# Optimization experiments

Measured on AMD Instinct MI355X. Metric: run time of the kernel, lower is better.

## Reference

```python
import jax, jax.numpy as jnp
from jax import lax
import numpy as np

B, C_IN, HW = 4096, 3, 32
D = 256          # feature/output dim
E = 16           # num experts
H = 1024         # expert hidden dim
K = 2            # top-k
NC = 1000        # num classes


def _conv(x, w, b):
    # x: NCHW, w: OIHW, stride 1, SAME padding
    y = lax.conv_general_dilated(x, w, (1, 1), 'SAME',
                                 dimension_numbers=('NCHW', 'OIHW', 'NCHW'))
    return y + b[None, :, None, None]


def _maxpool2(x):
    return lax.reduce_window(x, -jnp.inf, lax.max, (1, 1, 2, 2), (1, 1, 2, 2), 'VALID')


def setup_inputs() -> dict:
    key = jax.random.key(0)
    ks = jax.random.split(key, 16)
    s = lambda *sh: 1.0 / np.sqrt(sh[-2] if len(sh) > 1 else sh[0])
    inp = {
        'x':       jax.random.normal(ks[0], (B, C_IN, HW, HW), jnp.float32),
        'conv1_w': jax.random.normal(ks[1], (32, 3, 3, 3), jnp.float32) * 0.1,
        'conv1_b': jnp.zeros((32,), jnp.float32),
        'conv2_w': jax.random.normal(ks[2], (64, 32, 3, 3), jnp.float32) * 0.05,
        'conv2_b': jnp.zeros((64,), jnp.float32),
        'conv3_w': jax.random.normal(ks[3], (128, 64, 3, 3), jnp.float32) * 0.04,
        'conv3_b': jnp.zeros((128,), jnp.float32),
        'fc_w':    jax.random.normal(ks[4], (128 * 4 * 4, D), jnp.float32) * (1.0 / np.sqrt(2048)),
        'fc_b':    jnp.zeros((D,), jnp.float32),
        'gate_w':  jax.random.normal(ks[5], (D, E), jnp.float32) * (1.0 / np.sqrt(D)),
        'gate_b':  jnp.zeros((E,), jnp.float32),
        'e_w1':    jax.random.normal(ks[6], (E, D, H), jnp.float32) * (1.0 / np.sqrt(D)),
        'e_b1':    jnp.zeros((E, H), jnp.float32),
        'e_w2':    jax.random.normal(ks[7], (E, H, D), jnp.float32) * (1.0 / np.sqrt(H)),
        'e_b2':    jnp.zeros((E, D), jnp.float32),
        'ln_g':    jnp.ones((D,), jnp.float32),
        'ln_b':    jnp.zeros((D,), jnp.float32),
        'out_w':   jax.random.normal(ks[8], (D, NC), jnp.float32) * (1.0 / np.sqrt(D)),
        'out_b':   jnp.zeros((NC,), jnp.float32),
    }
    return inp


def reference(x, conv1_w, conv1_b, conv2_w, conv2_b, conv3_w, conv3_b,
              fc_w, fc_b, gate_w, gate_b, e_w1, e_b1, e_w2, e_b2,
              ln_g, ln_b, out_w, out_b):
    # --- CNN feature extractor: conv -> maxpool -> relu, x3 ---
    h = jax.nn.relu(_maxpool2(_conv(x, conv1_w, conv1_b)))   # [B,32,16,16]
    h = jax.nn.relu(_maxpool2(_conv(h, conv2_w, conv2_b)))   # [B,64,8,8]
    h = jax.nn.relu(_maxpool2(_conv(h, conv3_w, conv3_b)))   # [B,128,4,4]
    feat = h.reshape(h.shape[0], -1) @ fc_w + fc_b           # [B,D]

    # --- Gating: top-k softmax scattered into sparse [B,E] ---
    logits = feat @ gate_w + gate_b                          # [B,E]
    topk_vals, topk_idx = lax.top_k(logits, K)               # [B,K]
    gate_w_k = jax.nn.softmax(topk_vals, axis=-1)            # [B,K]
    gates = jnp.zeros_like(logits).at[jnp.arange(feat.shape[0])[:, None], topk_idx].set(gate_w_k)

    # --- Dense all-expert compute, masked combine (faithful to source) ---
    h1 = jax.nn.relu(jnp.einsum('bd,edh->beh', feat, e_w1) + e_b1[None])   # [B,E,H]
    eo = jnp.einsum('beh,ehd->bed', h1, e_w2) + e_b2[None]                 # [B,E,D]
    moe = jnp.einsum('be,bed->bd', gates, eo)                              # [B,D]

    D_i = gates.mean(axis=0)
    lb_loss = jnp.sum(D_i * jnp.log(D_i + 1e-8))

    # --- LayerNorm(residual) ---
    y = moe + feat
    mu = y.mean(-1, keepdims=True)
    var = y.var(-1, keepdims=True)
    y = (y - mu) / jnp.sqrt(var + 1e-5) * ln_g + ln_b

    out = y @ out_w + out_b                                   # [B,NC]
    return out, lb_loss
```

## Files before the change

kernel.cpp:

```cpp
#include <hip/hip_runtime.h>
#include <hip/hip_bf16.h>

typedef short bf16x8 __attribute__((ext_vector_type(8)));
typedef float f32x4 __attribute__((ext_vector_type(4)));

#define NB   4096
#define NEXP 16
#define DDIM 256
#define HDIM 1024
#define NCLS 1000

#define OFF_B    ((size_t)0)
#define OFF_P0   ((size_t)0)
#define OFF_P1   ((size_t)4194304)
#define OFF_W1TH ((size_t)8388608)
#define OFF_W1TL ((size_t)16777216)
#define OFF_W2TH ((size_t)25165824)
#define OFF_W2TL ((size_t)33554432)
#define OFF_WFCH ((size_t)41943040)
#define OFF_WFCL ((size_t)42991616)
#define OFF_P2   ((size_t)44040192)
#define OFF_P3   ((size_t)48234496)
#define OFF_OWH  ((size_t)52428800)
#define OFF_OWL  ((size_t)53477376)
#define OFF_CHH  ((size_t)67108864)
#define OFF_CHL  ((size_t)83886080)
#define OFF_WBL  ((size_t)67145728)
#define OFF_WA1H ((size_t)67182592)
#define OFF_WA1L ((size_t)67184640)
#define OFF_FEAT ((size_t)100663296)
#define OFF_WAL  ((size_t)100810752)
#define OFF_MOE  ((size_t)104857600)
#define OFF_CNT  ((size_t)109051904)
#define OFF_GSUM ((size_t)109051968)
#define OFF_LROW ((size_t)109052032)
#define OFF_LG   ((size_t)109314176)

__device__ inline unsigned short f2bf(float v) {
  __hip_bfloat16 h = __float2bfloat16(v);
  return *(unsigned short*)&h;
}
__device__ inline float bf2f(unsigned short u) {
  union { unsigned int i; float f; } c; c.i = ((unsigned int)u) << 16; return c.f;
}

__global__ __launch_bounds__(256) void k_wprep(
    const float* __restrict__ c1w, unsigned short* __restrict__ a1h, unsigned short* __restrict__ a1l,
    const float* __restrict__ c2w, unsigned short* __restrict__ b2h, unsigned short* __restrict__ b2l,
    const float* __restrict__ c3w, unsigned short* __restrict__ a3h, unsigned short* __restrict__ a3l) {
  int i = blockIdx.x*256 + threadIdx.x;
  if (i < 1024) {
    int k = i & 31, oc = i >> 5;
    float v = (k < 27) ? c1w[oc*27 + k] : 0.f;
    unsigned short h = f2bf(v);
    a1h[i] = h; a1l[i] = f2bf(v - bf2f(h));
  } else if (i < 19456) {
    int j = i - 1024;
    int ic = j & 31, rem = j >> 5;
    int oc = rem & 63, tap = rem >> 6;
    float v = c2w[(oc*32 + ic)*9 + tap];
    unsigned short h = f2bf(v);
    b2h[j] = h; b2l[j] = f2bf(v - bf2f(h));
  } else if (i < 93184) {
    int j = i - 19456;
    int ic = j & 63, rem = j >> 6;
    int oc = rem & 127, tap = rem >> 7;
    float v = c3w[(oc*64 + ic)*9 + tap];
    unsigned short h = f2bf(v);
    a3h[j] = h; a3l[j] = f2bf(v - bf2f(h));
  }
}

__device__ inline void pack_body(const float* __restrict__ in,
    unsigned short* __restrict__ oh, unsigned short* __restrict__ ol,
    int R, int C, int bx, int by, int e, int t, float (*tile)[65]) {
  const size_t eb = (size_t)e * R * C;
  const int c0 = bx*64, r0 = by*64;
  const int cc = t & 63, r4 = t >> 6;
  #pragma unroll
  for (int j = 0; j < 16; ++j) {
    int rr = r4 + j*4;
    tile[rr][cc] = in[eb + (size_t)(r0+rr)*C + c0 + cc];
  }
  __syncthreads();
  const int K32 = R >> 5;
  #pragma unroll
  for (int j = 0; j < 16; ++j) {
    int idx = t + j*256;
    int jin = idx & 7, lane = (idx >> 3) & 63, ksl = (idx >> 9) & 1, ntl = idx >> 10;
    int kl = ksl*32 + ((lane >> 4) << 3) + jin;
    int nl = ntl*16 + (lane & 15);
    float v = tile[kl][nl];
    unsigned short h = f2bf(v);
    size_t o = eb + ((size_t)(((c0 >> 4) + ntl)*K32 + (r0 >> 5) + ksl)*64 + lane)*8 + jin;
    oh[o] = h;
    ol[o] = f2bf(v - bf2f(h));
  }
}

__global__ __launch_bounds__(256) void k_packall(
    const float* __restrict__ ew1, unsigned short* __restrict__ w1th, unsigned short* __restrict__ w1tl,
    const float* __restrict__ ew2, unsigned short* __restrict__ w2th, unsigned short* __restrict__ w2tl,
    const float* __restrict__ fcw, unsigned short* __restrict__ wfh,  unsigned short* __restrict__ wfl,
    const float* __restrict__ ow,  unsigned short* __restrict__ owh,  unsigned short* __restrict__ owl) {
  __shared__ float tile[64][65];
  const int b = blockIdx.x;
  const int t = threadIdx.x;
  if (b < 1024) {
    int bx = b & 15, by = (b >> 4) & 3, e = b >> 6;
    pack_body(ew1, w1th, w1tl, 256, 1024, bx, by, e, t, tile);
  } else if (b < 2048) {
    int lb = b - 1024;
    int bx = lb & 3, by = (lb >> 2) & 15, e = lb >> 6;
    pack_body(ew2, w2th, w2tl, 1024, 256, bx, by, e, t, tile);
  } else if (b < 2176) {
    int lb = b - 2048;
    int bx = lb & 3, by = lb >> 2;
    pack_body(fcw, wfh, wfl, 2048, 256, bx, by, 0, t, tile);
  } else {
    int lb = b - 2176;
    int i = lb*256 + t;
    int j = i & 7, lane = (i >> 3) & 63, ks = (i >> 9) & 7, nt = i >> 12;
    int k = ks*32 + ((lane >> 4) << 3) + j;
    int n = nt*16 + (lane & 15);
    float v = (n < NCLS) ? ow[(size_t)k*NCLS + n] : 0.f;
    unsigned short h = f2bf(v);
    owh[i] = h;
    owl[i] = f2bf(v - bf2f(h));
  }
}

__global__ __launch_bounds__(512, 4) void k_conv12(const float* __restrict__ x,
    const unsigned short* __restrict__ wA1h, const unsigned short* __restrict__ wA1l,
    const float* __restrict__ b1,
    const unsigned short* __restrict__ wBh, const unsigned short* __restrict__ wBl,
    const float* __restrict__ b2, float* __restrict__ outB) {
  __shared__ unsigned int xsu[3*34*36];
  __shared__ __align__(16) unsigned short ishB[2][12960];
  __shared__ float bs1[32];
  __shared__ float bs2[64];
  const int t = threadIdx.x;
  const int img = blockIdx.x;
  for (int i = t; i < 3*34*36; i += 512) xsu[i] = 0u;
  {
    unsigned int* z = (unsigned int*)&ishB[0][0];
    for (int i = t; i < 2720; i += 512) {
      int plane = i / 1360, rem = i - plane*1360;
      int b = rem / 20, o = rem - b*20;
      int pl;
      if (b < 18)      pl = b;
      else if (b < 36) pl = 306 + (b - 18);
      else if (b < 52) pl = (b - 35) * 18;
      else             pl = (b - 51) * 18 + 17;
      z[plane*6480 + pl*20 + o] = 0u;
    }
  }
  __syncthreads();
  for (int i = t; i < 3072; i += 512) {
    int ic = i >> 10, rem = i & 1023, y = rem >> 5, xx = rem & 31;
    float v = x[(size_t)img*3072 + i];
    unsigned short h = f2bf(v);
    unsigned short l = f2bf(v - bf2f(h));
    xsu[ic*34*36 + (y+1)*36 + (xx+1)] = ((unsigned int)l << 16) | (unsigned int)h;
  }
  if (t < 32) bs1[t] = b1[t];
  else if (t >= 64 && t < 128) bs2[t-64] = b2[t-64];

  const int lane = t & 63, wvv = t >> 6;
  const int lr = lane & 15, lq = lane >> 4;

  const int oct1 = wvv & 1;
  const bf16x8 a1h = *(const bf16x8*)&wA1h[((oct1*16 + lr) << 5) + lq*8];
  const bf16x8 a1l = *(const bf16x8*)&wA1l[((oct1*16 + lr) << 5) + lq*8];

  int koff[8];
  #pragma unroll
  for (int j = 0; j < 8; ++j) {
    int k = lq*8 + j;
    if (k < 27) {
      int ic = k/9, tap = k - ic*9, dy = tap/3, dx = tap - dy*3;
      koff[j] = ic*34*36 + dy*36 + dx;
    } else koff[j] = -1;
  }
  __syncthreads();

  {
    const int rp  = wvv >> 1;
    const int ly0 = (rp >> 1) << 1;
    const int xh  = rp & 1;
    const int X   = xh*16 + lr;
    for (int ps = 0; ps < 8; ++ps) {
      const int baseA = (ps*4 + ly0)*36 + X;
      f32x4 aA = (f32x4){0.f,0.f,0.f,0.f}, aB = (f32x4){0.f,0.f,0.f,0.f};
      {
        union { unsigned int u[4]; bf16x8 v; } bh_, bl_;
        #pragma unroll
        for (int jj = 0; jj < 4; ++jj) {
          unsigned int e0 = (koff[2*jj]   >= 0) ? xsu[koff[2*jj]   + baseA] : 0u;
          unsigned int e1 = (koff[2*jj+1] >= 0) ? xsu[koff[2*jj+1] + baseA] : 0u;
          bh_.u[jj] = __builtin_amdgcn_perm(e1, e0, 0x05040100u);
          bl_.u[jj] = __builtin_amdgcn_perm(e1, e0, 0x07060302u);
        }
        aA = __builtin_amdgcn_mfma_f32_16x16x32_bf16(a1h, bh_.v, aA, 0, 0, 0);
        aA = __builtin_amdgcn_mfma_f32_16x16x32_bf16(a1h, bl_.v, aA, 0, 0, 0);
        aA = __builtin_amdgcn_mfma_f32_16x16x32_bf16(a1l, bh_.v, aA, 0, 0, 0);
      }
      {
        union { unsigned int u[4]; bf16x8 v; } bh_, bl_;
        #pragma unroll
        for (int jj = 0; jj < 4; ++jj) {
          unsigned int e0 = (koff[2*jj]   >= 0) ? xsu[koff[2*jj]   + baseA + 36] : 0u;
          unsigned int e1 = (koff[2*jj+1] >= 0) ? xsu[koff[2*jj+1] + baseA + 36] : 0u;
          bh_.u[jj] = __builtin_amdgcn_perm(e1, e0, 0x05040100u);
          bl_.u[jj] = __builtin_amdgcn_perm(e1, e0, 0x07060302u);
        }
        aB = __builtin_amdgcn_mfma_f32_16x16x32_bf16(a1h, bh_.v, aB, 0, 0, 0);
        aB = __builtin_amdgcn_mfma_f32_16x16x32_bf16(a1h, bl_.v, aB, 0, 0, 0);
        aB = __builtin_amdgcn_mfma_f32_16x16x32_bf16(a1l, bh_.v, aB, 0, 0, 0);
      }
      #pragma unroll
      for (int r = 0; r < 4; ++r) {
        float v = fmaxf(aA[r], aB[r]);
        v = fmaxf(v, __shfl_xor(v, 1, 64));
        if ((lr & 1) == 0) {
          int oc = oct1*16 + lq*4 + r;
          int Xp = xh*8 + (lr >> 1);
          int Yp = ps*2 + (ly0 >> 1);
          float m = fmaxf(v + bs1[oc], 0.f);
          unsigned short h = f2bf(m);
          unsigned short l = f2bf(m - bf2f(h));
          int pl = (Yp+1)*18 + (Xp+1);
          int us = (pl*5 + (oc >> 3))*8 + (oc & 7);
          ishB[0][us] = h; ishB[1][us] = l;
        }
      }
    }
  }
  __syncthreads();
  {
    const int mtp = (wvv & 1)*2;
    const int rq = wvv >> 1;
    f32x4 acc[2][4];
    #pragma unroll
    for (int i = 0; i < 2; ++i)
      #pragma unroll
      for (int j = 0; j < 4; ++j) acc[i][j] = (f32x4){0.f,0.f,0.f,0.f};
    #pragma unroll
    for (int tap = 0; tap < 9; ++tap) {
      const int off0 = ((tap*64 + mtp*16     + lr) << 5) + lq*8;
      const int off1 = ((tap*64 + (mtp+1)*16 + lr) << 5) + lq*8;
      bf16x8 ah0 = *(const bf16x8*)&wBh[off0];
      bf16x8 al0 = *(const bf16x8*)&wBl[off0];
      bf16x8 ah1 = *(const bf16x8*)&wBh[off1];
      bf16x8 al1 = *(const bf16x8*)&wBl[off1];
      const int dy = tap/3, dx = tap - dy*3;
      #pragma unroll
      for (int j = 0; j < 4; ++j) {
        int pl = (rq*4 + j + dy)*18 + lr + dx;
        int slot = pl*5 + lq;
        bf16x8 bh = *(const bf16x8*)&ishB[0][slot << 3];
        bf16x8 bl = *(const bf16x8*)&ishB[1][slot << 3];
        acc[0][j] = __builtin_amdgcn_mfma_f32_16x16x32_bf16(ah0, bh, acc[0][j], 0, 0, 0);
        acc[1][j] = __builtin_amdgcn_mfma_f32_16x16x32_bf16(ah1, bh, acc[1][j], 0, 0, 0);
        acc[0][j] = __builtin_amdgcn_mfma_f32_16x16x32_bf16(ah0, bl, acc[0][j], 0, 0, 0);
        acc[1][j] = __builtin_amdgcn_mfma_f32_16x16x32_bf16(ah1, bl, acc[1][j], 0, 0, 0);
        acc[0][j] = __builtin_amdgcn_mfma_f32_16x16x32_bf16(al0, bh, acc[0][j], 0, 0, 0);
        acc[1][j] = __builtin_amdgcn_mfma_f32_16x16x32_bf16(al1, bh, acc[1][j], 0, 0, 0);
      }
    }
    __syncthreads();
    float* ps2 = (float*)&ishB[0][0];
    #pragma unroll
    for (int m = 0; m < 2; ++m)
      #pragma unroll
      for (int k = 0; k < 2; ++k)
        #pragma unroll
        for (int r = 0; r < 4; ++r) {
          float v = fmaxf(acc[m][2*k][r], acc[m][2*k+1][r]);
          v = fmaxf(v, __shfl_xor(v, 1, 64));
          if ((lr & 1) == 0) {
            int oc = (mtp + m)*16 + lq*4 + r;
            int Y = rq*2 + k, X = lr >> 1;
            ps2[oc*65 + Y*8 + X] = fmaxf(v + bs2[oc], 0.f);
          }
        }
    __syncthreads();
    float* op = outB + (size_t)img*4096;
    #pragma unroll
    for (int jj = 0; jj < 8; ++jj) {
      int i = jj*512 + t;
      op[i] = ps2[(i >> 6)*65 + (i & 63)];
    }
  }
}

__global__ __launch_bounds__(256) void k_conv3(const float* __restrict__ inB,
    const unsigned short* __restrict__ wAh, const unsigned short* __restrict__ wAl,
    const float* __restrict__ bias,
    unsigned short* __restrict__ Chh, unsigned short* __restrict__ Chl) {
  __shared__ unsigned short ish[2][6400];
  const int t = threadIdx.x;
  const int img = blockIdx.x;
  {
    unsigned int* z = (unsigned int*)&ish[0][0];
    #pragma unroll
    for (int j = 0; j < 25; ++j) z[t + 256*j] = 0u;
  }
  __syncthreads();
  {
    const float* src = inB + (size_t)img*4096;
    #pragma unroll
    for (int j = 0; j < 16; ++j) {
      int f = t + 256*j;
      int ic = f >> 6, p = f & 63;
      int pl = ((p >> 3) + 1)*10 + (p & 7) + 1;
      float v = src[f];
      unsigned short h = f2bf(v);
      unsigned short l = f2bf(v - bf2f(h));
      int u = pl*64 + ic;
      int us = (((u >> 3) ^ (pl & 7)) << 3) | (u & 7);
      ish[0][us] = h; ish[1][us] = l;
    }
  }
  __syncthreads();

  const int lane = t & 63, wid = t >> 6;
  const int lr = lane & 15, lq = lane >> 4;
  const int mt0 = wid*2;
  const int yb = lr >> 3, xb = lr & 7;

  f32x4 acc[2][4];
  #pragma unroll
  for (int i = 0; i < 2; ++i)
    #pragma unroll
    for (int j = 0; j < 4; ++j) acc[i][j] = (f32x4){0.f,0.f,0.f,0.f};

  for (int tap = 0; tap < 9; ++tap) {
    const int dy = tap/3, dx = tap - dy*3;
    #pragma unroll
    for (int kc = 0; kc < 2; ++kc) {
      const int kb = kc*32 + lq*8;
      const int wbase = ((tap << 7) << 6) + kb;
      bf16x8 a0h = *(const bf16x8*)&wAh[wbase + ((mt0*16 + lr) << 6)];
      bf16x8 a0l = *(const bf16x8*)&wAl[wbase + ((mt0*16 + lr) << 6)];
      bf16x8 a1h = *(const bf16x8*)&wAh[wbase + (((mt0+1)*16 + lr) << 6)];
      bf16x8 a1l = *(const bf16x8*)&wAl[wbase + (((mt0+1)*16 + lr) << 6)];
      #pragma unroll
      for (int nt = 0; nt < 4; ++nt) {
        const int pl = (2*nt + yb + dy)*10 + xb + dx;
        const int u = pl*64 + kb;
        const int us = (((u >> 3) ^ (pl & 7)) << 3);
        bf16x8 bh = *(const bf16x8*)&ish[0][us];
        bf16x8 bl = *(const bf16x8*)&ish[1][us];
        acc[0][nt] = __builtin_amdgcn_mfma_f32_16x16x32_bf16(a0h, bh, acc[0][nt], 0, 0, 0);
        acc[0][nt] = __builtin_amdgcn_mfma_f32_16x16x32_bf16(a0h, bl, acc[0][nt], 0, 0, 0);
        acc[0][nt] = __builtin_amdgcn_mfma_f32_16x16x32_bf16(a0l, bh, acc[0][nt], 0, 0, 0);
        acc[1][nt] = __builtin_amdgcn_mfma_f32_16x16x32_bf16(a1h, bh, acc[1][nt], 0, 0, 0);
        acc[1][nt] = __builtin_amdgcn_mfma_f32_16x16x32_bf16(a1h, bl, acc[1][nt], 0, 0, 0);
        acc[1][nt] = __builtin_amdgcn_mfma_f32_16x16x32_bf16(a1l, bh, acc[1][nt], 0, 0, 0);
      }
    }
  }
  __syncthreads();
  float* stg = (float*)&ish[0][0];
  #pragma unroll
  for (int mtl = 0; mtl < 2; ++mtl)
    #pragma unroll
    for (int nt = 0; nt < 4; ++nt)
      #pragma unroll
      for (int r = 0; r < 4; ++r) {
        float v = acc[mtl][nt][r];
        v = fmaxf(v, __shfl_xor(v, 1, 64));
        v = fmaxf(v, __shfl_xor(v, 8, 64));
        if ((lane & 9) == 0) {
          int oc = (mt0 + mtl)*16 + lq*4 + r;
          int pix = nt*4 + (xb >> 1);
          stg[oc*17 + pix] = fmaxf(v + bias[oc], 0.f);
        }
      }
  __syncthreads();
  #pragma unroll
  for (int j = 0; j < 8; ++j) {
    int i = t + 256*j;
    float v = stg[(i >> 4)*17 + (i & 15)];
    unsigned short h = f2bf(v);
    Chh[(size_t)img*2048 + i] = h;
    Chl[(size_t)img*2048 + i] = f2bf(v - bf2f(h));
  }
}

__global__ __launch_bounds__(256) void k_fc(const unsigned short* __restrict__ Chh,
    const unsigned short* __restrict__ Chl,
    const unsigned short* __restrict__ wfh, const unsigned short* __restrict__ wfl,
    float* __restrict__ P0, float* __restrict__ P1,
    float* __restrict__ P2, float* __restrict__ P3) {
  const int t = threadIdx.x;
  const int r0 = blockIdx.x * 32;
  const int kq = blockIdx.z;
  float* __restrict__ P = (kq == 0) ? P0 : (kq == 1) ? P1 : (kq == 2) ? P2 : P3;
  const int lane = t & 63, wv = t >> 6;
  const int lr = lane & 15, lq = lane >> 4;
  f32x4 acc[2][4];
  #pragma unroll
  for (int i = 0; i < 2; ++i)
    #pragma unroll
    for (int j = 0; j < 4; ++j) acc[i][j] = (f32x4){0.f,0.f,0.f,0.f};
  bf16x8 ah[2], al[2], bh[4], bl[4];
  #pragma unroll
  for (int rt = 0; rt < 2; ++rt) {
    size_t ao = (size_t)(r0 + rt*16 + lr)*2048 + kq*512 + lq*8;
    ah[rt] = *(const bf16x8*)&Chh[ao];
    al[rt] = *(const bf16x8*)&Chl[ao];
  }
  #pragma unroll
  for (int nt = 0; nt < 4; ++nt) {
    size_t bo = ((size_t)((wv*4 + nt)*64 + kq*16)*64 + lane)*8;
    bh[nt] = *(const bf16x8*)&wfh[bo];
    bl[nt] = *(const bf16x8*)&wfl[bo];
  }
  #pragma unroll 4
  for (int ks = 0; ks < 16; ++ks) {
    bf16x8 nah[2], nal[2], nbh[4], nbl[4];
    if (ks < 15) {
      #pragma unroll
      for (int rt = 0; rt < 2; ++rt) {
        size_t ao = (size_t)(r0 + rt*16 + lr)*2048 + kq*512 + (ks+1)*32 + lq*8;
        nah[rt] = *(const bf16x8*)&Chh[ao];
        nal[rt] = *(const bf16x8*)&Chl[ao];
      }
      #pragma unroll
      for (int nt = 0; nt < 4; ++nt) {
        size_t bo = ((size_t)((wv*4 + nt)*64 + kq*16 + ks + 1)*64 + lane)*8;
        nbh[nt] = *(const bf16x8*)&wfh[bo];
        nbl[nt] = *(const bf16x8*)&wfl[bo];
      }
    }
    #pragma unroll
    for (int nt = 0; nt < 4; ++nt) {
      acc[0][nt] = __builtin_amdgcn_mfma_f32_16x16x32_bf16(ah[0], bh[nt], acc[0][nt], 0, 0, 0);
      acc[1][nt] = __builtin_amdgcn_mfma_f32_16x16x32_bf16(ah[1], bh[nt], acc[1][nt], 0, 0, 0);
      acc[0][nt] = __builtin_amdgcn_mfma_f32_16x16x32_bf16(ah[0], bl[nt], acc[0][nt], 0, 0, 0);
      acc[1][nt] = __builtin_amdgcn_mfma_f32_16x16x32_bf16(ah[1], bl[nt], acc[1][nt], 0, 0, 0);
      acc[0][nt] = __builtin_amdgcn_mfma_f32_16x16x32_bf16(al[0], bh[nt], acc[0][nt], 0, 0, 0);
      acc[1][nt] = __builtin_amdgcn_mfma_f32_16x16x32_bf16(al[1], bh[nt], acc[1][nt], 0, 0, 0);
    }
    if (ks < 15) {
      #pragma unroll
      for (int rt = 0; rt < 2; ++rt) { ah[rt] = nah[rt]; al[rt] = nal[rt]; }
      #pragma unroll
      for (int nt = 0; nt < 4; ++nt) { bh[nt] = nbh[nt]; bl[nt] = nbl[nt]; }
    }
  }
  #pragma unroll
  for (int rt = 0; rt < 2; ++rt)
    #pragma unroll
    for (int nt = 0; nt < 4; ++nt)
      #pragma unroll
      for (int r = 0; r < 4; ++r)
        P[(size_t)(r0 + rt*16 + lq*4 + r)*256 + (wv*4 + nt)*16 + lr] = acc[rt][nt][r];
}

__global__ __launch_bounds__(256) void k_gate(const float* __restrict__ P0,
    const float* __restrict__ P1, const float* __restrict__ P2, const float* __restrict__ P3,
    const float* __restrict__ fcb,
    const float* __restrict__ gw, const float* __restrict__ gb,
    float* __restrict__ feat, int* __restrict__ cnt, float* __restrict__ gsum,
    int* __restrict__ lrow, float* __restrict__ lg) {
  __shared__ float ft[16][256];
  __shared__ float lgs[16][16];
  __shared__ float gwl[4096];
  const int t = threadIdx.x;
  const int r0 = blockIdx.x * 16;
  for (int i = t; i < 4096; i += 256) gwl[i] = gw[i];
  float bb = fcb[t];
  #pragma unroll
  for (int r = 0; r < 16; ++r) {
    size_t off = (size_t)(r0+r)*256 + t;
    float v = P0[off] + P1[off] + P2[off] + P3[off] + bb;
    ft[r][t] = v;
    feat[off] = v;
  }
  __syncthreads();
  {
    int r = t >> 4, e = t & 15;
    float s = gb[e];
    for (int k = 0; k < 256; ++k) s = fmaf(ft[r][k], gwl[k*16 + e], s);
    lgs[r][e] = s;
  }
  __syncthreads();
  if (t < 16) {
    int r = t;
    float v1 = -3.402823e38f, v2 = -3.402823e38f;
    int i1 = 0, i2 = 0;
    for (int e = 0; e < 16; ++e) {
      float v = lgs[r][e];
      if (v > v1)      { v2 = v1; i2 = i1; v1 = v; i1 = e; }
      else if (v > v2) { v2 = v;  i2 = e; }
    }
    float ex = __expf(v2 - v1);
    float g1 = 1.f / (1.f + ex);
    float g2 = ex  / (1.f + ex);
    int row = r0 + r;
    int p1 = atomicAdd(&cnt[i1], 1); lrow[i1*4096 + p1] = row; lg[i1*4096 + p1] = g1;
    int p2 = atomicAdd(&cnt[i2], 1); lrow[i2*4096 + p2] = row; lg[i2*4096 + p2] = g2;
    atomicAdd(&gsum[i1], g1);
    atomicAdd(&gsum[i2], g2);
  }
}

__global__ __launch_bounds__(256) void k_moe(const float* __restrict__ feat,
    const unsigned short* __restrict__ w1th, const unsigned short* __restrict__ w1tl,
    const unsigned short* __restrict__ w2th, const unsigned short* __restrict__ w2tl,
    const float* __restrict__ eb1, const float* __restrict__ eb2,
    const int* __restrict__ cnt, const int* __restrict__ lrow, const float* __restrict__ lgw,
    float* __restrict__ moe) {
  const int e = blockIdx.y;
  const int n_e = cnt[e];
  const int start = blockIdx.x * 32;
  if (start >= n_e) return;
  const int c = blockIdx.z;
  const int n = min(32, n_e - start);
  __shared__ unsigned short fh[8192], fl[8192];
  __shared__ unsigned short h1h[4096], h1l[4096];
  __shared__ int   rws[32];
  __shared__ float gws[32];
  const int t = threadIdx.x;
  if (t < 32) {
    rws[t] = (t < n) ? lrow[e*4096 + start + t] : 0;
    gws[t] = (t < n) ? lgw[e*4096 + start + t] : 0.f;
  }
  __syncthreads();
  for (int j = 0; j < 32; ++j) {
    float v = (j < n) ? feat[(size_t)rws[j]*256 + t] : 0.f;
    unsigned short h = f2bf(v);
    int us = (j*32 + ((t >> 3) ^ (j & 7)))*8 + (t & 7);
    fh[us] = h; fl[us] = f2bf(v - bf2f(h));
  }
  const int lane = t & 63, wv = t >> 6;
  const int lr = lane & 15, lq = lane >> 4;
  const int rh = wv & 1, qh = wv >> 1;
  const int arow = rh*16 + lr;
  const int rsw = arow & 7;
  const size_t ewb = (size_t)e << 18;

  f32x4 acc2[8];
  #pragma unroll
  for (int i = 0; i < 8; ++i) acc2[i] = (f32x4){0.f,0.f,0.f,0.f};

  __syncthreads();

  {
    f32x4 acc1[4];
    #pragma unroll
    for (int i = 0; i < 4; ++i) acc1[i] = (f32x4){0.f,0.f,0.f,0.f};
    bf16x8 wbh[4], wbl[4];
    #pragma unroll
    for (int ht = 0; ht < 4; ++ht) {
      size_t bo = ewb + ((size_t)((c*8 + qh*4 + ht)*8 + 0)*64 + lane)*8;
      wbh[ht] = *(const bf16x8*)&w1th[bo];
      wbl[ht] = *(const bf16x8*)&w1tl[bo];
    }
    #pragma unroll
    for (int ks = 0; ks < 8; ++ks) {
      bf16x8 nbh[4], nbl[4];
      if (ks < 7) {
        #pragma unroll
        for (int ht = 0; ht < 4; ++ht) {
          size_t bo = ewb + ((size_t)((c*8 + qh*4 + ht)*8 + ks + 1)*64 + lane)*8;
          nbh[ht] = *(const bf16x8*)&w1th[bo];
          nbl[ht] = *(const bf16x8*)&w1tl[bo];
        }
      }
      int aoff = (arow*32 + ((ks*4 + lq) ^ rsw))*8;
      bf16x8 ah = *(const bf16x8*)&fh[aoff];
      bf16x8 al = *(const bf16x8*)&fl[aoff];
      #pragma unroll
      for (int ht = 0; ht < 4; ++ht) {
        acc1[ht] = __builtin_amdgcn_mfma_f32_16x16x32_bf16(ah, wbh[ht], acc1[ht], 0, 0, 0);
        acc1[ht] = __builtin_amdgcn_mfma_f32_16x16x32_bf16(ah, wbl[ht], acc1[ht], 0, 0, 0);
        acc1[ht] = __builtin_amdgcn_mfma_f32_16x16x32_bf16(al, wbh[ht], acc1[ht], 0, 0, 0);
      }
      if (ks < 7) {
        #pragma unroll
        for (int ht = 0; ht < 4; ++ht) { wbh[ht] = nbh[ht]; wbl[ht] = nbl[ht]; }
      }
    }
    __syncthreads();
    #pragma unroll
    for (int ht = 0; ht < 4; ++ht) {
      int hloc = qh*64 + ht*16 + lr;
      float bb = eb1[e*1024 + c*128 + hloc];
      #pragma unroll
      for (int r = 0; r < 4; ++r) {
        int orow = rh*16 + lq*4 + r;
        float v = fmaxf(acc1[ht][r] + bb, 0.f);
        unsigned short hh = f2bf(v);
        int us = (orow*16 + ((hloc >> 3) ^ (orow & 7)))*8 + (hloc & 7);
        h1h[us] = hh; h1l[us] = f2bf(v - bf2f(hh));
      }
    }
    __syncthreads();
    bf16x8 w2h[4], w2l[4];
    #pragma unroll
    for (int dt = 0; dt < 4; ++dt) {
      size_t bo = ewb + ((size_t)((qh*8 + dt)*32 + c*4 + 0)*64 + lane)*8;
      w2h[dt] = *(const bf16x8*)&w2th[bo];
      w2l[dt] = *(const bf16x8*)&w2tl[bo];
    }
    #pragma unroll
    for (int g = 0; g < 8; ++g) {
      const int ks = g >> 1, dth = (g & 1)*4;
      bf16x8 nh[4], nl[4];
      if (g < 7) {
        const int ks2 = (g+1) >> 1, dth2 = ((g+1) & 1)*4;
        #pragma unroll
        for (int dt = 0; dt < 4; ++dt) {
          size_t bo = ewb + ((size_t)((qh*8 + dth2 + dt)*32 + c*4 + ks2)*64 + lane)*8;
          nh[dt] = *(const bf16x8*)&w2th[bo];
          nl[dt] = *(const bf16x8*)&w2tl[bo];
        }
      }
      int aoff = (arow*16 + ((ks*4 + lq) ^ rsw))*8;
      bf16x8 ah = *(const bf16x8*)&h1h[aoff];
      bf16x8 al = *(const bf16x8*)&h1l[aoff];
      #pragma unroll
      for (int dt = 0; dt < 4; ++dt) {
        acc2[dth+dt] = __builtin_amdgcn_mfma_f32_16x16x32_bf16(ah, w2h[dt], acc2[dth+dt], 0, 0, 0);
        acc2[dth+dt] = __builtin_amdgcn_mfma_f32_16x16x32_bf16(ah, w2l[dt], acc2[dth+dt], 0, 0, 0);
        acc2[dth+dt] = __builtin_amdgcn_mfma_f32_16x16x32_bf16(al, w2h[dt], acc2[dth+dt], 0, 0, 0);
      }
      if (g < 7) {
        #pragma unroll
        for (int dt = 0; dt < 4; ++dt) { w2h[dt] = nh[dt]; w2l[dt] = nl[dt]; }
      }
    }
  }
  #pragma unroll
  for (int dt = 0; dt < 8; ++dt) {
    int d = qh*128 + dt*16 + lr;
    float b2 = (c == 0) ? eb2[e*256 + d] : 0.f;
    #pragma unroll
    for (int r = 0; r < 4; ++r) {
      int orow = rh*16 + lq*4 + r;
      if (orow < n)
        atomicAdd(&moe[(size_t)rws[orow]*256 + d], gws[orow]*(acc2[dt][r] + b2));
    }
  }
}

__global__ __launch_bounds__(256) void k_ln(const float* __restrict__ feat,
    const float* __restrict__ moe, const float* __restrict__ g, const float* __restrict__ bp,
    unsigned short* __restrict__ yh, unsigned short* __restrict__ yl,
    const float* __restrict__ gsum, float* __restrict__ out_lb) {
  const int r = blockIdx.x, t = threadIdx.x;
  if (r == NB) {
    if (t < 64) {
      float term = 0.f;
      if (t < 16) {
        float D = gsum[t] * (1.f/4096.f);
        term = D * logf(D + 1e-8f);
      }
      #pragma unroll
      for (int o = 8; o > 0; o >>= 1) term += __shfl_down(term, o, 64);
      if (t == 0) *out_lb = term;
    }
    return;
  }
  float v = moe[(size_t)r*256 + t] + feat[(size_t)r*256 + t];
  float s = v, q = v * v;
  #pragma unroll
  for (int o = 32; o > 0; o >>= 1) {
    s += __shfl_down(s, o, 64);
    q += __shfl_down(q, o, 64);
  }
  __shared__ float ss[4], qq[4];
  int wv = t >> 6;
  if ((t & 63) == 0) { ss[wv] = s; qq[wv] = q; }
  __syncthreads();
  float S = ss[0]+ss[1]+ss[2]+ss[3];
  float Q = qq[0]+qq[1]+qq[2]+qq[3];
  float mu  = S * (1.f/256.f);
  float var = Q * (1.f/256.f) - mu*mu;
  float inv = rsqrtf(var + 1e-5f);
  float y = (v - mu) * inv * g[t] + bp[t];
  unsigned short h = f2bf(y);
  yh[(size_t)r*256 + t] = h;
  yl[(size_t)r*256 + t] = f2bf(y - bf2f(h));
}

__global__ __launch_bounds__(256) void k_out(const unsigned short* __restrict__ yh,
    const unsigned short* __restrict__ yl,
    const unsigned short* __restrict__ owh, const unsigned short* __restrict__ owl,
    const float* __restrict__ ob, float* __restrict__ out) {
  const int t = threadIdx.x;
  const int r0 = blockIdx.x * 32;
  const int lane = t & 63, wv = t >> 6;
  const int lr = lane & 15, lq = lane >> 4;
  const int ntile = blockIdx.y*4 + wv;
  f32x4 acc[2];
  acc[0] = (f32x4){0.f,0.f,0.f,0.f};
  acc[1] = (f32x4){0.f,0.f,0.f,0.f};
  #pragma unroll
  for (int ks = 0; ks < 8; ++ks) {
    bf16x8 bh = *(const bf16x8*)&owh[((size_t)(ntile*8 + ks)*64 + lane)*8];
    bf16x8 bl = *(const bf16x8*)&owl[((size_t)(ntile*8 + ks)*64 + lane)*8];
    #pragma unroll
    for (int rt = 0; rt < 2; ++rt) {
      size_t ao = (size_t)(r0 + rt*16 + lr)*256 + ks*32 + lq*8;
      bf16x8 ah = *(const bf16x8*)&yh[ao];
      bf16x8 al = *(const bf16x8*)&yl[ao];
      acc[rt] = __builtin_amdgcn_mfma_f32_16x16x32_bf16(ah, bh, acc[rt], 0, 0, 0);
      acc[rt] = __builtin_amdgcn_mfma_f32_16x16x32_bf16(ah, bl, acc[rt], 0, 0, 0);
      acc[rt] = __builtin_amdgcn_mfma_f32_16x16x32_bf16(al, bh, acc[rt], 0, 0, 0);
    }
  }
  const int col = ntile*16 + lr;
  if (col < NCLS) {
    float bb = ob[col];
    #pragma unroll
    for (int rt = 0; rt < 2; ++rt)
      #pragma unroll
      for (int r = 0; r < 4; ++r)
        out[(size_t)(r0 + rt*16 + lq*4 + r)*NCLS + col] = acc[rt][r] + bb;
  }
}

extern "C" void kernel_launch(void* const* d_in, const int* in_sizes, int n_in,
                              void* d_out, int out_size, void* d_ws, size_t ws_size,
                              hipStream_t stream) {
  const float* x   = (const float*)d_in[0];
  const float* c1w = (const float*)d_in[1];
  const float* c1b = (const float*)d_in[2];
  const float* c2w = (const float*)d_in[3];
  const float* c2b = (const float*)d_in[4];
  const float* c3w = (const float*)d_in[5];
  const float* c3b = (const float*)d_in[6];
  const float* fcw = (const float*)d_in[7];
  const float* fcb = (const float*)d_in[8];
  const float* gw  = (const float*)d_in[9];
  const float* gb  = (const float*)d_in[10];
  const float* ew1 = (const float*)d_in[11];
  const float* eb1 = (const float*)d_in[12];
  const float* ew2 = (const float*)d_in[13];
  const float* eb2 = (const float*)d_in[14];
  const float* lng = (const float*)d_in[15];
  const float* lnb = (const float*)d_in[16];
  const float* ow  = (const float*)d_in[17];
  const float* ob  = (const float*)d_in[18];
  char* ws = (char*)d_ws;
  float* Bb   = (float*)(ws + OFF_B);
  float* P0   = (float*)(ws + OFF_P0);
  float* P1   = (float*)(ws + OFF_P1);
  float* P2   = (float*)(ws + OFF_P2);
  float* P3   = (float*)(ws + OFF_P3);
  unsigned short* Chh = (unsigned short*)(ws + OFF_CHH);
  unsigned short* Chl = (unsigned short*)(ws + OFF_CHL);
  unsigned short* wBh = (unsigned short*)(ws + OFF_CHH);
  unsigned short* wBl = (unsigned short*)(ws + OFF_WBL);
  unsigned short* wA1h = (unsigned short*)(ws + OFF_WA1H);
  unsigned short* wA1l = (unsigned short*)(ws + OFF_WA1L);
  unsigned short* wAh = (unsigned short*)(ws + OFF_FEAT);
  unsigned short* wAl = (unsigned short*)(ws + OFF_WAL);
  unsigned short* w1th = (unsigned short*)(ws + OFF_W1TH);
  unsigned short* w1tl = (unsigned short*)(ws + OFF_W1TL);
  unsigned short* w2th = (unsigned short*)(ws + OFF_W2TH);
  unsigned short* w2tl = (unsigned short*)(ws + OFF_W2TL);
  unsigned short* wfh = (unsigned short*)(ws + OFF_WFCH);
  unsigned short* wfl = (unsigned short*)(ws + OFF_WFCL);
  unsigned short* owph = (unsigned short*)(ws + OFF_OWH);
  unsigned short* owpl = (unsigned short*)(ws + OFF_OWL);
  unsigned short* yh = (unsigned short*)(ws + OFF_P0);
  unsigned short* yl = (unsigned short*)(ws + OFF_P1);
  float* feat = (float*)(ws + OFF_FEAT);
  float* moe  = (float*)(ws + OFF_MOE);
  int*   cnt  = (int*)(ws + OFF_CNT);
  float* gsum = (float*)(ws + OFF_GSUM);
  int*   lrow = (int*)(ws + OFF_LROW);
  float* lgv  = (float*)(ws + OFF_LG);
  float* outp = (float*)d_out;

  hipMemsetAsync(ws + OFF_MOE, 0, 4194304 + 128, stream);

  hipLaunchKernelGGL(k_wprep,  dim3(364),     dim3(256), 0, stream,
                     c1w, wA1h, wA1l, c2w, wBh, wBl, c3w, wAh, wAl);
  hipLaunchKernelGGL(k_conv12, dim3(4096),    dim3(512), 0, stream, x, wA1h, wA1l, c1b, wBh, wBl, c2b, Bb);
  hipLaunchKernelGGL(k_conv3,  dim3(4096),    dim3(256), 0, stream, Bb, wAh, wAl, c3b, Chh, Chl);
  hipLaunchKernelGGL(k_packall, dim3(3200),   dim3(256), 0, stream,
                     ew1, w1th, w1tl, ew2, w2th, w2tl, fcw, wfh, wfl, ow, owph, owpl);
  hipLaunchKernelGGL(k_fc,     dim3(128, 1, 4), dim3(256), 0, stream, Chh, Chl, wfh, wfl, P0, P1, P2, P3);
  hipLaunchKernelGGL(k_gate,   dim3(256),     dim3(256), 0, stream, P0, P1, P2, P3, fcb, gw, gb,
                     feat, cnt, gsum, lrow, lgv);
  hipLaunchKernelGGL(k_moe,    dim3(128, 16, 8), dim3(256), 0, stream, feat, w1th, w1tl, w2th, w2tl,
                     eb1, eb2, cnt, lrow, lgv, moe);
  hipLaunchKernelGGL(k_ln,     dim3(4097),    dim3(256), 0, stream, feat, moe, lng, lnb, yh, yl,
                     gsum, outp + (size_t)NB*NCLS);
  hipLaunchKernelGGL(k_out,    dim3(128, 16), dim3(256), 0, stream, yh, yl, owph, owpl, ob, outp);
}
```

Baseline: 744.2 us.

## Fuse weight packing into conv3 launch, drop conv1 bounds checks, prefetch in k_out

When the workspace is large enough, weight packing blocks move to new workspace offsets and run as extra blocks of the conv3 launch, so one kernel launch disappears and the packing overlaps with conv3. The conv1 im2col now points padded K entries at a zeroed LDS region, which removes the per-element branch. The output GEMM software-prefetches the next k-slice of A and B operands into registers. Each is independent, and the fused path depends on the workspace size the harness provides.

```diff
diff --git a/kernel.cpp b/kernel.cpp
--- a/kernel.cpp
+++ b/kernel.cpp
@@ -35,6 +35,15 @@
 #define OFF_GSUM ((size_t)109051968)
 #define OFF_LROW ((size_t)109052032)
 #define OFF_LG   ((size_t)109314176)
+#define OFF2_W1TH ((size_t)109600768)
+#define OFF2_W1TL ((size_t)117989376)
+#define OFF2_W2TH ((size_t)126377984)
+#define OFF2_W2TL ((size_t)134766592)
+#define OFF2_WFCH ((size_t)143155200)
+#define OFF2_WFCL ((size_t)144203776)
+#define OFF2_OWH  ((size_t)145252352)
+#define OFF2_OWL  ((size_t)146300928)
+#define WS_BIG    ((size_t)147349504)
 
 __device__ inline unsigned short f2bf(float v) {
   __hip_bfloat16 h = __float2bfloat16(v);
@@ -98,14 +107,11 @@
   }
 }
 
-__global__ __launch_bounds__(256) void k_packall(
+__device__ inline void pack_dispatch(int b, int t, float (*tile)[65],
     const float* __restrict__ ew1, unsigned short* __restrict__ w1th, unsigned short* __restrict__ w1tl,
     const float* __restrict__ ew2, unsigned short* __restrict__ w2th, unsigned short* __restrict__ w2tl,
     const float* __restrict__ fcw, unsigned short* __restrict__ wfh,  unsigned short* __restrict__ wfl,
     const float* __restrict__ ow,  unsigned short* __restrict__ owh,  unsigned short* __restrict__ owl) {
-  __shared__ float tile[64][65];
-  const int b = blockIdx.x;
-  const int t = threadIdx.x;
   if (b < 1024) {
     int bx = b & 15, by = (b >> 4) & 3, e = b >> 6;
     pack_body(ew1, w1th, w1tl, 256, 1024, bx, by, e, t, tile);
@@ -130,18 +136,28 @@
   }
 }
 
+__global__ __launch_bounds__(256) void k_packall(
+    const float* __restrict__ ew1, unsigned short* __restrict__ w1th, unsigned short* __restrict__ w1tl,
+    const float* __restrict__ ew2, unsigned short* __restrict__ w2th, unsigned short* __restrict__ w2tl,
+    const float* __restrict__ fcw, unsigned short* __restrict__ wfh,  unsigned short* __restrict__ wfl,
+    const float* __restrict__ ow,  unsigned short* __restrict__ owh,  unsigned short* __restrict__ owl) {
+  __shared__ float tile[64][65];
+  pack_dispatch(blockIdx.x, threadIdx.x, tile,
+                ew1, w1th, w1tl, ew2, w2th, w2tl, fcw, wfh, wfl, ow, owh, owl);
+}
+
 __global__ __launch_bounds__(512, 4) void k_conv12(const float* __restrict__ x,
     const unsigned short* __restrict__ wA1h, const unsigned short* __restrict__ wA1l,
     const float* __restrict__ b1,
     const unsigned short* __restrict__ wBh, const unsigned short* __restrict__ wBl,
     const float* __restrict__ b2, float* __restrict__ outB) {
-  __shared__ unsigned int xsu[3*34*36];
+  __shared__ unsigned int xsu[3*34*36 + 1152];
   __shared__ __align__(16) unsigned short ishB[2][12960];
   __shared__ float bs1[32];
   __shared__ float bs2[64];
   const int t = threadIdx.x;
   const int img = blockIdx.x;
-  for (int i = t; i < 3*34*36; i += 512) xsu[i] = 0u;
+  for (int i = t; i < 3*34*36 + 1152; i += 512) xsu[i] = 0u;
   {
     unsigned int* z = (unsigned int*)&ishB[0][0];
     for (int i = t; i < 2720; i += 512) {
@@ -180,7 +196,7 @@
     if (k < 27) {
       int ic = k/9, tap = k - ic*9, dy = tap/3, dx = tap - dy*3;
       koff[j] = ic*34*36 + dy*36 + dx;
-    } else koff[j] = -1;
+    } else koff[j] = 3*34*36;
   }
   __syncthreads();
 
@@ -196,8 +212,8 @@
         union { unsigned int u[4]; bf16x8 v; } bh_, bl_;
         #pragma unroll
         for (int jj = 0; jj < 4; ++jj) {
-          unsigned int e0 = (koff[2*jj]   >= 0) ? xsu[koff[2*jj]   + baseA] : 0u;
-          unsigned int e1 = (koff[2*jj+1] >= 0) ? xsu[koff[2*jj+1] + baseA] : 0u;
+          unsigned int e0 = xsu[koff[2*jj]   + baseA];
+          unsigned int e1 = xsu[koff[2*jj+1] + baseA];
           bh_.u[jj] = __builtin_amdgcn_perm(e1, e0, 0x05040100u);
           bl_.u[jj] = __builtin_amdgcn_perm(e1, e0, 0x07060302u);
         }
@@ -209,8 +225,8 @@
         union { unsigned int u[4]; bf16x8 v; } bh_, bl_;
         #pragma unroll
         for (int jj = 0; jj < 4; ++jj) {
-          unsigned int e0 = (koff[2*jj]   >= 0) ? xsu[koff[2*jj]   + baseA + 36] : 0u;
-          unsigned int e1 = (koff[2*jj+1] >= 0) ? xsu[koff[2*jj+1] + baseA + 36] : 0u;
+          unsigned int e0 = xsu[koff[2*jj]   + baseA + 36];
+          unsigned int e1 = xsu[koff[2*jj+1] + baseA + 36];
           bh_.u[jj] = __builtin_amdgcn_perm(e1, e0, 0x05040100u);
           bl_.u[jj] = __builtin_amdgcn_perm(e1, e0, 0x07060302u);
         }
@@ -297,9 +313,19 @@
 __global__ __launch_bounds__(256) void k_conv3(const float* __restrict__ inB,
     const unsigned short* __restrict__ wAh, const unsigned short* __restrict__ wAl,
     const float* __restrict__ bias,
-    unsigned short* __restrict__ Chh, unsigned short* __restrict__ Chl) {
+    unsigned short* __restrict__ Chh, unsigned short* __restrict__ Chl,
+    const float* __restrict__ ew1, unsigned short* __restrict__ w1th, unsigned short* __restrict__ w1tl,
+    const float* __restrict__ ew2, unsigned short* __restrict__ w2th, unsigned short* __restrict__ w2tl,
+    const float* __restrict__ fcw, unsigned short* __restrict__ wfh,  unsigned short* __restrict__ wfl,
+    const float* __restrict__ ow,  unsigned short* __restrict__ owh,  unsigned short* __restrict__ owl) {
   __shared__ unsigned short ish[2][6400];
   const int t = threadIdx.x;
+  if (blockIdx.x >= 4096) {
+    float (*tile)[65] = (float(*)[65])&ish[0][0];
+    pack_dispatch(blockIdx.x - 4096, t, tile,
+                  ew1, w1th, w1tl, ew2, w2th, w2tl, fcw, wfh, wfl, ow, owh, owl);
+    return;
+  }
   const int img = blockIdx.x;
   {
     unsigned int* z = (unsigned int*)&ish[0][0];
@@ -700,18 +726,42 @@
   f32x4 acc[2];
   acc[0] = (f32x4){0.f,0.f,0.f,0.f};
   acc[1] = (f32x4){0.f,0.f,0.f,0.f};
+  bf16x8 bh, bl, ah[2], al[2];
+  {
+    size_t bo = ((size_t)(ntile*8)*64 + lane)*8;
+    bh = *(const bf16x8*)&owh[bo];
+    bl = *(const bf16x8*)&owl[bo];
+  }
+  #pragma unroll
+  for (int rt = 0; rt < 2; ++rt) {
+    size_t ao = (size_t)(r0 + rt*16 + lr)*256 + lq*8;
+    ah[rt] = *(const bf16x8*)&yh[ao];
+    al[rt] = *(const bf16x8*)&yl[ao];
+  }
   #pragma unroll
   for (int ks = 0; ks < 8; ++ks) {
-    bf16x8 bh = *(const bf16x8*)&owh[((size_t)(ntile*8 + ks)*64 + lane)*8];
-    bf16x8 bl = *(const bf16x8*)&owl[((size_t)(ntile*8 + ks)*64 + lane)*8];
+    bf16x8 nbh, nbl, nah[2], nal[2];
+    if (ks < 7) {
+      size_t bo = ((size_t)(ntile*8 + ks + 1)*64 + lane)*8;
+      nbh = *(const bf16x8*)&owh[bo];
+      nbl = *(const bf16x8*)&owl[bo];
+      #pragma unroll
+      for (int rt = 0; rt < 2; ++rt) {
+        size_t ao = (size_t)(r0 + rt*16 + lr)*256 + (ks+1)*32 + lq*8;
+        nah[rt] = *(const bf16x8*)&yh[ao];
+        nal[rt] = *(const bf16x8*)&yl[ao];
+      }
+    }
     #pragma unroll
     for (int rt = 0; rt < 2; ++rt) {
-      size_t ao = (size_t)(r0 + rt*16 + lr)*256 + ks*32 + lq*8;
-      bf16x8 ah = *(const bf16x8*)&yh[ao];
-      bf16x8 al = *(const bf16x8*)&yl[ao];
-      acc[rt] = __builtin_amdgcn_mfma_f32_16x16x32_bf16(ah, bh, acc[rt], 0, 0, 0);
-      acc[rt] = __builtin_amdgcn_mfma_f32_16x16x32_bf16(ah, bl, acc[rt], 0, 0, 0);
-      acc[rt] = __builtin_amdgcn_mfma_f32_16x16x32_bf16(al, bh, acc[rt], 0, 0, 0);
+      acc[rt] = __builtin_amdgcn_mfma_f32_16x16x32_bf16(ah[rt], bh, acc[rt], 0, 0, 0);
+      acc[rt] = __builtin_amdgcn_mfma_f32_16x16x32_bf16(ah[rt], bl, acc[rt], 0, 0, 0);
+      acc[rt] = __builtin_amdgcn_mfma_f32_16x16x32_bf16(al[rt], bh, acc[rt], 0, 0, 0);
+    }
+    if (ks < 7) {
+      bh = nbh; bl = nbl;
+      #pragma unroll
+      for (int rt = 0; rt < 2; ++rt) { ah[rt] = nah[rt]; al[rt] = nal[rt]; }
     }
   }
   const int col = ntile*16 + lr;
@@ -748,6 +798,16 @@
   const float* ow  = (const float*)d_in[17];
   const float* ob  = (const float*)d_in[18];
   char* ws = (char*)d_ws;
+  const bool bigws = ws_size >= WS_BIG;
+  const size_t oW1TH = bigws ? OFF2_W1TH : OFF_W1TH;
+  const size_t oW1TL = bigws ? OFF2_W1TL : OFF_W1TL;
+  const size_t oW2TH = bigws ? OFF2_W2TH : OFF_W2TH;
+  const size_t oW2TL = bigws ? OFF2_W2TL : OFF_W2TL;
+  const size_t oWFCH = bigws ? OFF2_WFCH : OFF_WFCH;
+  const size_t oWFCL = bigws ? OFF2_WFCL : OFF_WFCL;
+  const size_t oOWH  = bigws ? OFF2_OWH  : OFF_OWH;
+  const size_t oOWL  = bigws ? OFF2_OWL  : OFF_OWL;
+
   float* Bb   = (float*)(ws + OFF_B);
   float* P0   = (float*)(ws + OFF_P0);
   float* P1   = (float*)(ws + OFF_P1);
@@ -761,14 +821,14 @@
   unsigned short* wA1l = (unsigned short*)(ws + OFF_WA1L);
   unsigned short* wAh = (unsigned short*)(ws + OFF_FEAT);
   unsigned short* wAl = (unsigned short*)(ws + OFF_WAL);
-  unsigned short* w1th = (unsigned short*)(ws + OFF_W1TH);
-  unsigned short* w1tl = (unsigned short*)(ws + OFF_W1TL);
-  unsigned short* w2th = (unsigned short*)(ws + OFF_W2TH);
-  unsigned short* w2tl = (unsigned short*)(ws + OFF_W2TL);
-  unsigned short* wfh = (unsigned short*)(ws + OFF_WFCH);
-  unsigned short* wfl = (unsigned short*)(ws + OFF_WFCL);
-  unsigned short* owph = (unsigned short*)(ws + OFF_OWH);
-  unsigned short* owpl = (unsigned short*)(ws + OFF_OWL);
+  unsigned short* w1th = (unsigned short*)(ws + oW1TH);
+  unsigned short* w1tl = (unsigned short*)(ws + oW1TL);
+  unsigned short* w2th = (unsigned short*)(ws + oW2TH);
+  unsigned short* w2tl = (unsigned short*)(ws + oW2TL);
+  unsigned short* wfh = (unsigned short*)(ws + oWFCH);
+  unsigned short* wfl = (unsigned short*)(ws + oWFCL);
+  unsigned short* owph = (unsigned short*)(ws + oOWH);
+  unsigned short* owpl = (unsigned short*)(ws + oOWL);
   unsigned short* yh = (unsigned short*)(ws + OFF_P0);
   unsigned short* yl = (unsigned short*)(ws + OFF_P1);
   float* feat = (float*)(ws + OFF_FEAT);
@@ -784,9 +844,12 @@
   hipLaunchKernelGGL(k_wprep,  dim3(364),     dim3(256), 0, stream,
                      c1w, wA1h, wA1l, c2w, wBh, wBl, c3w, wAh, wAl);
   hipLaunchKernelGGL(k_conv12, dim3(4096),    dim3(512), 0, stream, x, wA1h, wA1l, c1b, wBh, wBl, c2b, Bb);
-  hipLaunchKernelGGL(k_conv3,  dim3(4096),    dim3(256), 0, stream, Bb, wAh, wAl, c3b, Chh, Chl);
-  hipLaunchKernelGGL(k_packall, dim3(3200),   dim3(256), 0, stream,
+  hipLaunchKernelGGL(k_conv3,  dim3(bigws ? 7296 : 4096), dim3(256), 0, stream,
+                     Bb, wAh, wAl, c3b, Chh, Chl,
                      ew1, w1th, w1tl, ew2, w2th, w2tl, fcw, wfh, wfl, ow, owph, owpl);
+  if (!bigws)
+    hipLaunchKernelGGL(k_packall, dim3(3200), dim3(256), 0, stream,
+                       ew1, w1th, w1tl, ew2, w2th, w2tl, fcw, wfh, wfl, ow, owph, owpl);
   hipLaunchKernelGGL(k_fc,     dim3(128, 1, 4), dim3(256), 0, stream, Chh, Chl, wfh, wfl, P0, P1, P2, P3);
   hipLaunchKernelGGL(k_gate,   dim3(256),     dim3(256), 0, stream, P0, P1, P2, P3, fcb, gw, gb,
                      feat, cnt, gsum, lrow, lgv);
```

Measured after the change: 730.1 us. About the same (-1.9%).
